# Optimization experiments

Measured on AMD Instinct MI355X. Metric: run time of the kernel, lower is better.

The kernel has to match this reference:

```python
import jax, jax.numpy as jnp
import numpy as np

LN_EPS = 1e-12  # BERT LayerNorm eps


def _layernorm(x, g, b):
    mu = jnp.mean(x, axis=-1, keepdims=True)
    var = jnp.mean(jnp.square(x - mu), axis=-1, keepdims=True)
    return (x - mu) * jax.lax.rsqrt(var + LN_EPS) * g + b


def setup_inputs() -> dict:
    key = jax.random.key(0)
    B, M, D, H, dh, R, Ro, Rf, F = 4, 2048, 768, 12, 64, 32, 256, 256, 3072
    ks = iter(jax.random.split(key, 32))
    n = lambda shape, s=0.02: jax.random.normal(next(ks), shape, jnp.float32) * s
    return {
        'x': jax.random.normal(next(ks), (B, M, D), jnp.float32),
        'mask': jnp.zeros((B, M), jnp.float32),  # HF-style additive mask
        'Pq': n((H, D, R)), 'Vq': n((H, R, dh)), 'bq': n((1, H, 1, dh)),
        'Pk': n((H, D, R)), 'Vk': n((H, R, dh)), 'bk': n((1, H, 1, dh)),
        'Pv': n((H, D, R)), 'Vv': n((H, R, dh)), 'bv': n((1, H, 1, dh)),
        'Uo': n((D, Ro)), 'Vo': n((Ro, D)), 'bo_attn': jnp.zeros((D,), jnp.float32),
        'U1': n((D, Rf)), 'V1': n((Rf, F)), 'b1': jnp.zeros((F,), jnp.float32),
        'U2': n((F, Rf)), 'V2': n((Rf, D)), 'b2': jnp.zeros((D,), jnp.float32),
        'ln1_g': jnp.ones((D,), jnp.float32), 'ln1_b': jnp.zeros((D,), jnp.float32),
        'ln2_g': jnp.ones((D,), jnp.float32), 'ln2_b': jnp.zeros((D,), jnp.float32),
    }


def reference(x, mask, Pq, Vq, bq, Pk, Vk, bk, Pv, Vv, bv,
              Uo, Vo, bo_attn, U1, V1, b1, U2, V2, b2,
              ln1_g, ln1_b, ln2_g, ln2_b):
    B, M, D = x.shape
    H, dh = Pq.shape[0], Vq.shape[2]
    # low-rank per-head Q/K/V: x @ P (bhmr) then @ V (bhmd) + bias
    q = jnp.einsum('bhmr,hrd->bhmd', jnp.einsum('bmd,hdr->bhmr', x, Pq), Vq) + bq
    k = jnp.einsum('bhmr,hrd->bhmd', jnp.einsum('bmd,hdr->bhmr', x, Pk), Vk) + bk
    v = jnp.einsum('bhmr,hrd->bhmd', jnp.einsum('bmd,hdr->bhmr', x, Pv), Vv) + bv
    # attention (flash_svd_attention math: scaled dot-product + additive mask)
    scores = jnp.einsum('bhmd,bhnd->bhmn', q, k) / jnp.sqrt(jnp.float32(dh))
    scores = scores + mask[:, None, None, :]
    attn = jnp.einsum('bhmn,bhnd->bhmd', jax.nn.softmax(scores, axis=-1), v)
    attn = attn.transpose(0, 2, 1, 3).reshape(B, M, D)
    # low-rank output projection + residual + LN1
    x1 = _layernorm(x + (attn @ Uo) @ Vo + bo_attn, ln1_g, ln1_b)
    # low-rank FFN (BERT intermediate: exact GELU)
    mid = x1 @ U1
    y = (jax.nn.gelu(mid @ V1 + b1, approximate=False) @ U2) @ V2 + b2
    return _layernorm(x1 + y, ln2_g, ln2_b)
```

## Files before the change

kernel.cpp:

```cpp
#include <hip/hip_runtime.h>
#include <hip/hip_bf16.h>
#include <math.h>

typedef __hip_bfloat16 bf16;
typedef __attribute__((ext_vector_type(8))) short short8;
typedef __attribute__((ext_vector_type(4))) short short4v;
typedef __attribute__((ext_vector_type(4))) float f32x4;

__device__ __forceinline__ float to_f(float x) { return x; }
__device__ __forceinline__ float to_f(bf16 x) { return __bfloat162float(x); }

template <typename T> __device__ __forceinline__ T from_f(float x);
template <> __device__ __forceinline__ float from_f<float>(float x) { return x; }
template <> __device__ __forceinline__ bf16 from_f<bf16>(float x) { return __float2bfloat16(x); }

__device__ __forceinline__ float gelu_exact(float x) {
    return 0.5f * x * (1.0f + erff(x * 0.70710678118654752f));
}

#define GLD_LDS16(g, l)                                               \
    __builtin_amdgcn_global_load_lds(                                 \
        (const __attribute__((address_space(1))) void*)(g),           \
        (__attribute__((address_space(3))) void*)(l), 16, 0, 0)

__global__ __launch_bounds__(256) void build_w_qkv_lds(const float* __restrict__ Pq,
                                                       const float* __restrict__ Vq,
                                                       const float* __restrict__ Pk,
                                                       const float* __restrict__ Vk,
                                                       const float* __restrict__ Pv,
                                                       const float* __restrict__ Vv,
                                                       bf16* __restrict__ Wt) {
    const int dt = blockIdx.x;
    const int h = blockIdx.y;
    const int which = blockIdx.z;
    const float* P = (which == 0) ? Pq : (which == 1) ? Pk : Pv;
    const float* V = (which == 0) ? Vq : (which == 1) ? Vk : Vv;
    __shared__ __align__(16) float Ps[128][36];
    __shared__ __align__(16) float Vs[32][64];
    __shared__ __align__(16) unsigned int Ot[64][68];
    const int tid = threadIdx.x;

    const float* pbase = P + ((size_t)h * 768 + dt * 128) * 32;
#pragma unroll
    for (int i = 0; i < 4; i++) {
        int idx = tid + i * 256;
        float4 v4 = ((const float4*)pbase)[idx];
        *(float4*)&Ps[idx >> 3][(idx & 7) * 4] = v4;
    }
    const float* vbase = V + (size_t)h * 2048;
#pragma unroll
    for (int i = 0; i < 2; i++) {
        int idx = tid + i * 256;
        ((float4*)&Vs[0][0])[idx] = ((const float4*)vbase)[idx];
    }
    __syncthreads();

    const int e = tid & 63, w = tid >> 6;
    float vreg[32];
#pragma unroll
    for (int r = 0; r < 32; r++) vreg[r] = Vs[r][e];

#pragma unroll
    for (int dp = 0; dp < 16; dp++) {
        const int d0 = w * 32 + dp * 2;
        float a0 = 0.f, a1 = 0.f;
#pragma unroll
        for (int r4 = 0; r4 < 8; r4++) {
            float4 p0 = *(const float4*)&Ps[d0][r4 * 4];
            float4 p1 = *(const float4*)&Ps[d0 + 1][r4 * 4];
            a0 += p0.x * vreg[r4 * 4] + p0.y * vreg[r4 * 4 + 1] + p0.z * vreg[r4 * 4 + 2] + p0.w * vreg[r4 * 4 + 3];
            a1 += p1.x * vreg[r4 * 4] + p1.y * vreg[r4 * 4 + 1] + p1.z * vreg[r4 * 4 + 2] + p1.w * vreg[r4 * 4 + 3];
        }
        unsigned int lo = (unsigned int)(unsigned short)__builtin_bit_cast(short, from_f<bf16>(a0));
        unsigned int hi = (unsigned int)(unsigned short)__builtin_bit_cast(short, from_f<bf16>(a1));
        Ot[e][w * 16 + dp] = lo | (hi << 16);
    }
    __syncthreads();

    const int erow = tid >> 2, c0 = (tid & 3) * 16;
    bf16* dst = Wt + ((size_t)which * 768 + h * 64 + erow) * 768 + dt * 128 + c0 * 2;
    *(uint4*)(dst) = *(const uint4*)&Ot[erow][c0];
    *(uint4*)(dst + 8) = *(const uint4*)&Ot[erow][c0 + 4];
    *(uint4*)(dst + 16) = *(const uint4*)&Ot[erow][c0 + 8];
    *(uint4*)(dst + 24) = *(const uint4*)&Ot[erow][c0 + 12];
}

__global__ __launch_bounds__(256) void cast_transpose_t(const float* __restrict__ in,
                                                        bf16* __restrict__ out,
                                                        int R, int Cc) {
    __shared__ float t[32][33];
    const int r0 = blockIdx.x * 32, c0 = blockIdx.y * 32;
    const int tx = threadIdx.x & 31, ty = threadIdx.x >> 5;
#pragma unroll
    for (int i = 0; i < 4; i++)
        t[ty + i * 8][tx] = in[(size_t)(r0 + ty + i * 8) * Cc + c0 + tx];
    __syncthreads();
#pragma unroll
    for (int i = 0; i < 4; i++)
        out[(size_t)(c0 + ty + i * 8) * R + r0 + tx] = from_f<bf16>(t[tx][ty + i * 8]);
}

__global__ __launch_bounds__(256) void cast_f32_bf16(const float* __restrict__ in,
                                                     bf16* __restrict__ out, int n4) {
    int t = blockIdx.x * 256 + threadIdx.x;
    if (t >= n4) return;
    float4 v = ((const float4*)in)[t];
    bf16 tmp[4] = {from_f<bf16>(v.x), from_f<bf16>(v.y), from_f<bf16>(v.z), from_f<bf16>(v.w)};
    ((short4v*)out)[t] = *(short4v*)tmp;
}

__global__ __launch_bounds__(256) void pack_bias_mask(const float* __restrict__ bq,
                                                      const float* __restrict__ bk,
                                                      const float* __restrict__ bv,
                                                      const float* __restrict__ mask,
                                                      float* __restrict__ bias_out,
                                                      float* __restrict__ mask2) {
    int t = blockIdx.x * 256 + threadIdx.x;
    if (t < 768) {
        bias_out[t] = bq[t];
        bias_out[768 + t] = bk[t];
        bias_out[1536 + t] = bv[t];
    }
    int m = t - 768;
    if (m >= 0 && m < 8192) mask2[m] = mask[m] * 1.44269504088896f;
}

template <typename TOUT, int EPI>
__global__ __launch_bounds__(256) void gemm_mfma(const bf16* __restrict__ A,
                                                 const bf16* __restrict__ Bt,
                                                 const float* __restrict__ bias,
                                                 TOUT* __restrict__ C,
                                                 int M, int N, int K) {
    __shared__ __align__(16) bf16 As[128 * 32];
    __shared__ __align__(16) bf16 Bs[128 * 32];
    const int tid = threadIdx.x;
    const int w = tid >> 6, lane = tid & 63;
    const int l = lane & 15, quad = lane >> 4;
    const int wm = w >> 1, wn = w & 1;
    const int m0 = blockIdx.x * 128, n0 = blockIdx.y * 128;

    const int r_in = lane >> 2;
    const int slot = lane & 3;
    const int rA0 = 2 * w * 16 + r_in, rA1 = rA0 + 16;
    const int q0 = slot ^ ((rA0 >> 1) & 3);
    const int q1 = slot ^ ((rA1 >> 1) & 3);
    const bf16* a0 = A + (size_t)(m0 + rA0) * K + q0 * 8;
    const bf16* a1 = A + (size_t)(m0 + rA1) * K + q1 * 8;
    const bf16* b0 = Bt + (size_t)(n0 + rA0) * K + q0 * 8;
    const bf16* b1 = Bt + (size_t)(n0 + rA1) * K + q1 * 8;
    bf16* lA0 = As + 2 * w * 512;
    bf16* lA1 = lA0 + 512;
    bf16* lB0 = Bs + 2 * w * 512;
    bf16* lB1 = lB0 + 512;

    const int swz = (quad ^ ((l >> 1) & 3)) * 8;
    f32x4 acc[4][4] = {};

    for (int k0 = 0; k0 < K; k0 += 32) {
        GLD_LDS16(a0 + k0, lA0);
        GLD_LDS16(a1 + k0, lA1);
        GLD_LDS16(b0 + k0, lB0);
        GLD_LDS16(b1 + k0, lB1);
        __syncthreads();
        short8 af[4], bfr[4];
#pragma unroll
        for (int mt = 0; mt < 4; mt++)
            af[mt] = *(const short8*)&As[(wm * 64 + mt * 16 + l) * 32 + swz];
#pragma unroll
        for (int nt = 0; nt < 4; nt++)
            bfr[nt] = *(const short8*)&Bs[(wn * 64 + nt * 16 + l) * 32 + swz];
#pragma unroll
        for (int mt = 0; mt < 4; mt++)
#pragma unroll
            for (int nt = 0; nt < 4; nt++)
                acc[mt][nt] = __builtin_amdgcn_mfma_f32_16x16x32_bf16(af[mt], bfr[nt], acc[mt][nt], 0, 0, 0);
        __syncthreads();
    }

    float bs[4];
#pragma unroll
    for (int nt = 0; nt < 4; nt++)
        bs[nt] = bias ? bias[n0 + wn * 64 + nt * 16 + l] : 0.f;
#pragma unroll
    for (int mt = 0; mt < 4; mt++) {
#pragma unroll
        for (int nt = 0; nt < 4; nt++) {
            const int col = n0 + wn * 64 + nt * 16 + l;
#pragma unroll
            for (int r = 0; r < 4; r++) {
                const int row = m0 + wm * 64 + mt * 16 + quad * 4 + r;
                float val = acc[mt][nt][r] + bs[nt];
                if (EPI == 1) val = gelu_exact(val);
                C[(size_t)row * N + col] = from_f<TOUT>(val);
            }
        }
    }
}

template <typename TOUT, int EPI>
__global__ __launch_bounds__(256) void gemm_mfma64(const bf16* __restrict__ A,
                                                   const bf16* __restrict__ Bt,
                                                   const float* __restrict__ bias,
                                                   TOUT* __restrict__ C,
                                                   int M, int N, int K) {
    __shared__ __align__(16) bf16 As[64 * 32];
    __shared__ __align__(16) bf16 Bs[64 * 32];
    const int tid = threadIdx.x;
    const int w = tid >> 6, lane = tid & 63;
    const int l = lane & 15, quad = lane >> 4;
    const int wm = w >> 1, wn = w & 1;
    const int m0 = blockIdx.x * 64, n0 = blockIdx.y * 64;

    const int cid = tid;
    const int srow = cid >> 2, slot = cid & 3;
    const int gq = slot ^ ((srow >> 1) & 3);
    const bf16* ag = A + (size_t)(m0 + srow) * K + gq * 8;
    const bf16* bg = Bt + (size_t)(n0 + srow) * K + gq * 8;
    bf16* lA = As + w * 512;
    bf16* lB = Bs + w * 512;

    f32x4 acc[2][2] = {};

    for (int k0 = 0; k0 < K; k0 += 32) {
        GLD_LDS16(ag + k0, lA);
        GLD_LDS16(bg + k0, lB);
        __syncthreads();
        short8 af[2], bfr[2];
#pragma unroll
        for (int mt = 0; mt < 2; mt++) {
            const int row = wm * 32 + mt * 16 + l;
            af[mt] = *(const short8*)&As[row * 32 + (quad ^ ((row >> 1) & 3)) * 8];
        }
#pragma unroll
        for (int nt = 0; nt < 2; nt++) {
            const int row = wn * 32 + nt * 16 + l;
            bfr[nt] = *(const short8*)&Bs[row * 32 + (quad ^ ((row >> 1) & 3)) * 8];
        }
#pragma unroll
        for (int mt = 0; mt < 2; mt++)
#pragma unroll
            for (int nt = 0; nt < 2; nt++)
                acc[mt][nt] = __builtin_amdgcn_mfma_f32_16x16x32_bf16(af[mt], bfr[nt], acc[mt][nt], 0, 0, 0);
        __syncthreads();
    }

#pragma unroll
    for (int mt = 0; mt < 2; mt++) {
#pragma unroll
        for (int nt = 0; nt < 2; nt++) {
            const int col = n0 + wn * 32 + nt * 16 + l;
            const float bsv = bias ? bias[col] : 0.f;
#pragma unroll
            for (int r = 0; r < 4; r++) {
                const int row = m0 + wm * 32 + mt * 16 + quad * 4 + r;
                float val = acc[mt][nt][r] + bsv;
                if (EPI == 1) val = gelu_exact(val);
                C[(size_t)row * N + col] = from_f<TOUT>(val);
            }
        }
    }
}

__global__ __launch_bounds__(256) void transpose_v(const bf16* __restrict__ qkv,
                                                   bf16* __restrict__ vt) {
    __shared__ __align__(16) bf16 t[64][72];
    const int m0 = blockIdx.x * 64;
    const int h = blockIdx.y;
    const int tid = threadIdx.x;
    const int r = tid >> 2, c0 = (tid & 3) * 16;
    {
        const size_t g = (size_t)(m0 + r) * 2304 + 1536 + h * 64 + c0;
        *(short8*)&t[r][c0] = *(const short8*)(qkv + g);
        *(short8*)&t[r][c0 + 8] = *(const short8*)(qkv + g + 8);
    }
    __syncthreads();
    const int b = m0 >> 11, mm = m0 & 2047;
    const int e = tid >> 2, mi0 = (tid & 3) * 16;
    bf16 tmp[16];
#pragma unroll
    for (int j = 0; j < 16; j++) tmp[j] = t[mi0 + j][e];
    bf16* dst = vt + (((size_t)b * 12 + h) * 64 + e) * 2048 + mm + mi0;
    *(short8*)dst = *(short8*)&tmp[0];
    *(short8*)(dst + 8) = *(short8*)&tmp[8];
}

__global__ __launch_bounds__(256, 4) void flash_attn_mfma(const bf16* __restrict__ qkv,
                                                          const bf16* __restrict__ vt,
                                                          const float* __restrict__ mask2,
                                                          bf16* __restrict__ opart0,
                                                          bf16* __restrict__ opart1,
                                                          float* __restrict__ lpart) {
    const int qt = blockIdx.x, h = blockIdx.y;
    const int b = blockIdx.z >> 1, kh = blockIdx.z & 1;
    const int tid = threadIdx.x;
    const int w = tid >> 6, lane = tid & 63;
    const int l = lane & 15, quad = lane >> 4;

    __shared__ __align__(16) bf16 Ks[2][64 * 64];
    __shared__ __align__(16) bf16 Vs[2][64 * 64];
    __shared__ __align__(16) bf16 Ps[4 * 32 * 64];

    const float C1 = 0.125f * 1.44269504088896f;

    short8 qf[2][2];
#pragma unroll
    for (int mt = 0; mt < 2; mt++) {
        const int qrow = qt * 128 + w * 32 + mt * 16 + l;
        const bf16* qp = qkv + ((size_t)b * 2048 + qrow) * 2304 + h * 64 + quad * 8;
        qf[mt][0] = *(const short8*)qp;
        qf[mt][1] = *(const short8*)(qp + 32);
    }

    short8 ones;
#pragma unroll
    for (int i = 0; i < 8; i++) ones[i] = (short)0x3F80;

    f32x4 of[2][4] = {};
    f32x4 lacc[2] = {};
    bf16* Pw = Ps + w * 2048;

    auto stage = [&](int kc, int buf) {
#pragma unroll
        for (int i = 0; i < 2; i++) {
            const int cid = (w * 2 + i) * 64 + lane;
            const int row = cid >> 3, slot = cid & 7;
            const int gq = slot ^ (row & 7);
            const bf16* kp = qkv + ((size_t)b * 2048 + kc + row) * 2304 + 768 + h * 64 + gq * 8;
            GLD_LDS16(kp, &Ks[buf][(size_t)cid * 8]);
            const bf16* vp = vt + (((size_t)b * 12 + h) * 64 + row) * 2048 + kc + gq * 8;
            GLD_LDS16(vp, &Vs[buf][(size_t)cid * 8]);
        }
    };

    const int kc0 = kh * 1024;
    int cur = 0;
    stage(kc0, 0);

    for (int it = 0; it < 16; it++) {
        const int kc = kc0 + it * 64;
        __syncthreads();
        float4 mrow[4];
#pragma unroll
        for (int nt = 0; nt < 4; nt++)
            mrow[nt] = *(const float4*)&mask2[(size_t)b * 2048 + kc + nt * 16 + quad * 4];
        if (it < 15) stage(kc + 64, cur ^ 1);

        const bf16* Kc = Ks[cur];
        const bf16* Vc = Vs[cur];

        f32x4 st[2][4];
#pragma unroll
        for (int nt = 0; nt < 4; nt++) {
            const int rb = (nt * 16 + l) * 64;
            short8 kf0 = *(const short8*)&Kc[rb + ((quad) ^ (l & 7)) * 8];
            short8 kf1 = *(const short8*)&Kc[rb + ((4 + quad) ^ (l & 7)) * 8];
#pragma unroll
            for (int mt = 0; mt < 2; mt++) {
                f32x4 a = {};
                a = __builtin_amdgcn_mfma_f32_16x16x32_bf16(kf0, qf[mt][0], a, 0, 0, 0);
                a = __builtin_amdgcn_mfma_f32_16x16x32_bf16(kf1, qf[mt][1], a, 0, 0, 0);
                st[mt][nt] = a;
            }
        }

#pragma unroll
        for (int mt = 0; mt < 2; mt++) {
#pragma unroll
            for (int nt = 0; nt < 4; nt++) {
                const float* mg = (const float*)&mrow[nt];
                float p0 = exp2f(fmaf(st[mt][nt][0], C1, mg[0]));
                float p1 = exp2f(fmaf(st[mt][nt][1], C1, mg[1]));
                float p2 = exp2f(fmaf(st[mt][nt][2], C1, mg[2]));
                float p3 = exp2f(fmaf(st[mt][nt][3], C1, mg[3]));
                unsigned d0 = __builtin_amdgcn_perm(__builtin_bit_cast(unsigned, p1),
                                                    __builtin_bit_cast(unsigned, p0), 0x07060302u);
                unsigned d1 = __builtin_amdgcn_perm(__builtin_bit_cast(unsigned, p3),
                                                    __builtin_bit_cast(unsigned, p2), 0x07060302u);
                const int slot8 = (2 * nt + (quad >> 1)) ^ (l & 7);
                uint2 u = {d0, d1};
                *(uint2*)&Pw[(mt * 16 + l) * 64 + slot8 * 8 + (quad & 1) * 4] = u;
            }
        }

        short8 pa[2][2];
#pragma unroll
        for (int mt = 0; mt < 2; mt++)
#pragma unroll
            for (int ks = 0; ks < 2; ks++)
                pa[mt][ks] = *(const short8*)&Pw[(mt * 16 + l) * 64 + ((ks * 4 + quad) ^ (l & 7)) * 8];

#pragma unroll
        for (int mt = 0; mt < 2; mt++) {
            lacc[mt] = __builtin_amdgcn_mfma_f32_16x16x32_bf16(pa[mt][0], ones, lacc[mt], 0, 0, 0);
            lacc[mt] = __builtin_amdgcn_mfma_f32_16x16x32_bf16(pa[mt][1], ones, lacc[mt], 0, 0, 0);
        }

#pragma unroll
        for (int nt = 0; nt < 4; nt++) {
            const int rb = (nt * 16 + l) * 64;
            short8 vf0 = *(const short8*)&Vc[rb + ((quad) ^ (l & 7)) * 8];
            short8 vf1 = *(const short8*)&Vc[rb + ((4 + quad) ^ (l & 7)) * 8];
#pragma unroll
            for (int mt = 0; mt < 2; mt++) {
                of[mt][nt] = __builtin_amdgcn_mfma_f32_16x16x32_bf16(pa[mt][0], vf0, of[mt][nt], 0, 0, 0);
                of[mt][nt] = __builtin_amdgcn_mfma_f32_16x16x32_bf16(pa[mt][1], vf1, of[mt][nt], 0, 0, 0);
            }
        }
        cur ^= 1;
    }

#pragma unroll
    for (int mt = 0; mt < 2; mt++) {
        if (l == 0) {
#pragma unroll
            for (int r = 0; r < 4; r++)
                lpart[(((size_t)kh * 4 + b) * 12 + h) * 2048 + qt * 128 + w * 32 + mt * 16 + quad * 4 + r] =
                    lacc[mt][r];
        }
    }

    bf16* op = kh ? opart1 : opart0;
#pragma unroll
    for (int mt = 0; mt < 2; mt++) {
#pragma unroll
        for (int r = 0; r < 4; r++) {
            const int row = qt * 128 + w * 32 + mt * 16 + quad * 4 + r;
#pragma unroll
            for (int nt = 0; nt < 4; nt++)
                op[((size_t)b * 2048 + row) * 768 + h * 64 + nt * 16 + l] =
                    from_f<bf16>(of[mt][nt][r]);
        }
    }
}

__global__ __launch_bounds__(256) void attn_combine(const bf16* __restrict__ o0,
                                                    const bf16* __restrict__ o1,
                                                    const float* __restrict__ lp,
                                                    bf16* __restrict__ outp) {
    const int t = blockIdx.x * 256 + threadIdx.x;
    const int col4 = t % 192;
    const int row = t / 192;
    const int b = row >> 11, m = row & 2047;
    const int h = col4 >> 4;
    const float l0 = lp[((size_t)b * 12 + h) * 2048 + m];
    const float l1 = lp[((size_t)(4 + b) * 12 + h) * 2048 + m];
    const float iv = 1.f / (l0 + l1);
    short4v a = ((const short4v*)o0)[t];
    short4v c = ((const short4v*)o1)[t];
    bf16 r[4];
#pragma unroll
    for (int i = 0; i < 4; i++) {
        float f = to_f(__builtin_bit_cast(bf16, a[i])) + to_f(__builtin_bit_cast(bf16, c[i]));
        r[i] = from_f<bf16>(f * iv);
    }
    ((short4v*)outp)[t] = *(short4v*)r;
}

template <typename TIN, typename TADD, typename TOUT>
__global__ __launch_bounds__(256) void ln_kernel(const TIN* __restrict__ base,
                                                 const TADD* __restrict__ add,
                                                 const float* __restrict__ gamma,
                                                 const float* __restrict__ beta,
                                                 TOUT* __restrict__ out) {
    const int row = blockIdx.x;
    const int tid = threadIdx.x;
    __shared__ float red[4];
    const size_t o = (size_t)row * 768;
    float v[3];
#pragma unroll
    for (int i = 0; i < 3; i++) {
        int d = tid + i * 256;
        v[i] = to_f(base[o + d]) + to_f(add[o + d]);
    }
    float s = v[0] + v[1] + v[2];
#pragma unroll
    for (int off = 32; off > 0; off >>= 1) s += __shfl_down(s, off, 64);
    const int wave = tid >> 6, lane = tid & 63;
    if (lane == 0) red[wave] = s;
    __syncthreads();
    float mu = (red[0] + red[1] + red[2] + red[3]) * (1.0f / 768.0f);
    float d0 = v[0] - mu, d1 = v[1] - mu, d2 = v[2] - mu;
    float sq = d0 * d0 + d1 * d1 + d2 * d2;
    __syncthreads();
#pragma unroll
    for (int off = 32; off > 0; off >>= 1) sq += __shfl_down(sq, off, 64);
    if (lane == 0) red[wave] = sq;
    __syncthreads();
    float var = (red[0] + red[1] + red[2] + red[3]) * (1.0f / 768.0f);
    float rs = rsqrtf(var + 1e-12f);
#pragma unroll
    for (int i = 0; i < 3; i++) {
        int d = tid + i * 256;
        float y = (v[i] - mu) * rs * gamma[d] + beta[d];
        out[o + d] = from_f<TOUT>(y);
    }
}

extern "C" void kernel_launch(void* const* d_in, const int* in_sizes, int n_in,
                              void* d_out, int out_size, void* d_ws, size_t ws_size,
                              hipStream_t stream) {
    const float* x    = (const float*)d_in[0];
    const float* mask = (const float*)d_in[1];
    const float* Pq = (const float*)d_in[2];
    const float* Vq = (const float*)d_in[3];
    const float* bq = (const float*)d_in[4];
    const float* Pk = (const float*)d_in[5];
    const float* Vk = (const float*)d_in[6];
    const float* bk = (const float*)d_in[7];
    const float* Pv = (const float*)d_in[8];
    const float* Vv = (const float*)d_in[9];
    const float* bv = (const float*)d_in[10];
    const float* Uo = (const float*)d_in[11];
    const float* Vo = (const float*)d_in[12];
    const float* bo = (const float*)d_in[13];
    const float* U1 = (const float*)d_in[14];
    const float* V1 = (const float*)d_in[15];
    const float* b1 = (const float*)d_in[16];
    const float* U2 = (const float*)d_in[17];
    const float* V2 = (const float*)d_in[18];
    const float* b2 = (const float*)d_in[19];
    const float* g1 = (const float*)d_in[20];
    const float* be1 = (const float*)d_in[21];
    const float* g2 = (const float*)d_in[22];
    const float* be2 = (const float*)d_in[23];

    char* p = (char*)d_ws;
    bf16* Wqkv_t = (bf16*)p;            p += (size_t)2304 * 768 * 2;
    bf16* Wo_t   = (bf16*)p;            p += (size_t)768 * 768 * 2;
    bf16* U1t    = (bf16*)p;            p += (size_t)256 * 768 * 2;
    bf16* V1t    = (bf16*)p;            p += (size_t)3072 * 256 * 2;
    bf16* U2t    = (bf16*)p;            p += (size_t)256 * 3072 * 2;
    bf16* V2t    = (bf16*)p;            p += (size_t)768 * 256 * 2;
    float* bias_qkv = (float*)p;        p += (size_t)2304 * 4;
    float* mask2 = (float*)p;           p += (size_t)8192 * 4;
    bf16* xb     = (bf16*)p;
    bf16* x1b    = xb;                  p += (size_t)8192 * 768 * 2;
    bf16* qkv    = (bf16*)p;
    bf16* gbuf   = qkv;                 p += (size_t)8192 * 2304 * 2;
    bf16* vtb    = (bf16*)p;            p += (size_t)8192 * 768 * 2;
    bf16* attnb  = (bf16*)p;
    bf16* t2     = attnb;               p += (size_t)8192 * 768 * 2;
    char* regR   = p;                   p += (size_t)8192 * 768 * 4;
    bf16* t1     = (bf16*)p;            p += (size_t)8192 * 256 * 2;
    bf16* Vot = (bf16*)regR;
    bf16* Uob = Vot + (size_t)768 * 256;
    bf16* opart1 = (bf16*)regR;
    float* lpart = (float*)(regR + (size_t)8192 * 768 * 2);
    bf16* y1b = (bf16*)regR;
    bf16* y2b = (bf16*)(regR + (size_t)8192 * 768 * 2);

    build_w_qkv_lds<<<dim3(6, 12, 3), 256, 0, stream>>>(Pq, Vq, Pk, Vk, Pv, Vv, Wqkv_t);
    cast_transpose_t<<<dim3(8, 24), 256, 0, stream>>>(Vo, Vot, 256, 768);
    cast_f32_bf16<<<192, 256, 0, stream>>>(Uo, Uob, 768 * 256 / 4);
    gemm_mfma<bf16, 0><<<dim3(6, 6), 256, 0, stream>>>(Vot, Uob, nullptr, Wo_t, 768, 768, 256);
    cast_transpose_t<<<dim3(24, 8), 256, 0, stream>>>(U1, U1t, 768, 256);
    cast_transpose_t<<<dim3(8, 96), 256, 0, stream>>>(V1, V1t, 256, 3072);
    cast_transpose_t<<<dim3(96, 8), 256, 0, stream>>>(U2, U2t, 3072, 256);
    cast_transpose_t<<<dim3(8, 24), 256, 0, stream>>>(V2, V2t, 256, 768);
    pack_bias_mask<<<35, 256, 0, stream>>>(bq, bk, bv, mask, bias_qkv, mask2);
    cast_f32_bf16<<<6144, 256, 0, stream>>>(x, xb, 8192 * 768 / 4);

    gemm_mfma<bf16, 0><<<dim3(64, 18), 256, 0, stream>>>(xb, Wqkv_t, bias_qkv, qkv, 8192, 2304, 768);

    transpose_v<<<dim3(128, 12), 256, 0, stream>>>(qkv, vtb);

    flash_attn_mfma<<<dim3(16, 12, 8), 256, 0, stream>>>(qkv, vtb, mask2, attnb, opart1, lpart);
    attn_combine<<<6144, 256, 0, stream>>>(attnb, opart1, lpart, attnb);

    gemm_mfma<bf16, 0><<<dim3(64, 6), 256, 0, stream>>>(attnb, Wo_t, bo, y1b, 8192, 768, 768);

    ln_kernel<float, bf16, bf16><<<8192, 256, 0, stream>>>(x, y1b, g1, be1, x1b);

    gemm_mfma64<bf16, 0><<<dim3(128, 4), 256, 0, stream>>>(x1b, U1t, nullptr, t1, 8192, 256, 768);

    gemm_mfma<bf16, 1><<<dim3(64, 24), 256, 0, stream>>>(t1, V1t, b1, gbuf, 8192, 3072, 256);

    gemm_mfma64<bf16, 0><<<dim3(128, 4), 256, 0, stream>>>(gbuf, U2t, nullptr, t2, 8192, 256, 3072);

    gemm_mfma<bf16, 0><<<dim3(64, 6), 256, 0, stream>>>(t2, V2t, b2, y2b, 8192, 768, 256);

    ln_kernel<bf16, bf16, float><<<8192, 256, 0, stream>>>(x1b, y2b, g2, be2, (float*)d_out);
}
```

Baseline: 430.6 us.

## Fold softmax scale into Q weights, batch weight transposes, trim attention overhead

```diff
diff --git a/kernel.cpp b/kernel.cpp
--- a/kernel.cpp
+++ b/kernel.cpp
@@ -6,6 +6,9 @@
 typedef __attribute__((ext_vector_type(8))) short short8;
 typedef __attribute__((ext_vector_type(4))) short short4v;
 typedef __attribute__((ext_vector_type(4))) float f32x4;
+
+#define C1F 0.18033688011112042f
+#define LOG2E 1.44269504088896f
 
 __device__ __forceinline__ float to_f(float x) { return x; }
 __device__ __forceinline__ float to_f(bf16 x) { return __bfloat162float(x); }
@@ -35,6 +38,7 @@
     const int which = blockIdx.z;
     const float* P = (which == 0) ? Pq : (which == 1) ? Pk : Pv;
     const float* V = (which == 0) ? Vq : (which == 1) ? Vk : Vv;
+    const float scale = (which == 0) ? C1F : 1.0f;
     __shared__ __align__(16) float Ps[128][36];
     __shared__ __align__(16) float Vs[32][64];
     __shared__ __align__(16) unsigned int Ot[64][68];
@@ -71,6 +75,8 @@
             a0 += p0.x * vreg[r4 * 4] + p0.y * vreg[r4 * 4 + 1] + p0.z * vreg[r4 * 4 + 2] + p0.w * vreg[r4 * 4 + 3];
             a1 += p1.x * vreg[r4 * 4] + p1.y * vreg[r4 * 4 + 1] + p1.z * vreg[r4 * 4 + 2] + p1.w * vreg[r4 * 4 + 3];
         }
+        a0 *= scale;
+        a1 *= scale;
         unsigned int lo = (unsigned int)(unsigned short)__builtin_bit_cast(short, from_f<bf16>(a0));
         unsigned int hi = (unsigned int)(unsigned short)__builtin_bit_cast(short, from_f<bf16>(a1));
         Ot[e][w * 16 + dp] = lo | (hi << 16);
@@ -85,19 +91,44 @@
     *(uint4*)(dst + 24) = *(const uint4*)&Ot[erow][c0 + 12];
 }
 
+__device__ __forceinline__ void ct_tile(const float* in, bf16* out, int R, int Cc,
+                                        int r0, int c0, int tx, int ty) {
+    __shared__ float t[32][33];
+#pragma unroll
+    for (int i = 0; i < 4; i++)
+        t[ty + i * 8][tx] = in[(size_t)(r0 + ty + i * 8) * Cc + c0 + tx];
+    __syncthreads();
+#pragma unroll
+    for (int i = 0; i < 4; i++)
+        out[(size_t)(c0 + ty + i * 8) * R + r0 + tx] = from_f<bf16>(t[tx][ty + i * 8]);
+}
+
 __global__ __launch_bounds__(256) void cast_transpose_t(const float* __restrict__ in,
                                                         bf16* __restrict__ out,
                                                         int R, int Cc) {
-    __shared__ float t[32][33];
-    const int r0 = blockIdx.x * 32, c0 = blockIdx.y * 32;
-    const int tx = threadIdx.x & 31, ty = threadIdx.x >> 5;
-#pragma unroll
-    for (int i = 0; i < 4; i++)
-        t[ty + i * 8][tx] = in[(size_t)(r0 + ty + i * 8) * Cc + c0 + tx];
-    __syncthreads();
-#pragma unroll
-    for (int i = 0; i < 4; i++)
-        out[(size_t)(c0 + ty + i * 8) * R + r0 + tx] = from_f<bf16>(t[tx][ty + i * 8]);
+    ct_tile(in, out, R, Cc, blockIdx.x * 32, blockIdx.y * 32,
+            threadIdx.x & 31, threadIdx.x >> 5);
+}
+
+__global__ __launch_bounds__(256) void cast_transpose_batch(const float* __restrict__ U1,
+                                                            const float* __restrict__ V1,
+                                                            const float* __restrict__ U2,
+                                                            const float* __restrict__ V2,
+                                                            bf16* __restrict__ U1t,
+                                                            bf16* __restrict__ V1t,
+                                                            bf16* __restrict__ U2t,
+                                                            bf16* __restrict__ V2t) {
+    int t = blockIdx.x;
+    const float* in;
+    bf16* out;
+    int R, Cc;
+    if (t < 192) { in = U1; out = U1t; R = 768; Cc = 256; }
+    else if (t < 960) { t -= 192; in = V1; out = V1t; R = 256; Cc = 3072; }
+    else if (t < 1728) { t -= 960; in = U2; out = U2t; R = 3072; Cc = 256; }
+    else { t -= 1728; in = V2; out = V2t; R = 256; Cc = 768; }
+    const int tpr = Cc >> 5;
+    ct_tile(in, out, R, Cc, (t / tpr) * 32, (t % tpr) * 32,
+            threadIdx.x & 31, threadIdx.x >> 5);
 }
 
 __global__ __launch_bounds__(256) void cast_f32_bf16(const float* __restrict__ in,
@@ -117,12 +148,12 @@
                                                       float* __restrict__ mask2) {
     int t = blockIdx.x * 256 + threadIdx.x;
     if (t < 768) {
-        bias_out[t] = bq[t];
+        bias_out[t] = bq[t] * C1F;
         bias_out[768 + t] = bk[t];
         bias_out[1536 + t] = bv[t];
     }
     int m = t - 768;
-    if (m >= 0 && m < 8192) mask2[m] = mask[m] * 1.44269504088896f;
+    if (m >= 0 && m < 8192) mask2[m] = mask[m] * LOG2E;
 }
 
 template <typename TOUT, int EPI>
@@ -298,9 +329,7 @@
 
     __shared__ __align__(16) bf16 Ks[2][64 * 64];
     __shared__ __align__(16) bf16 Vs[2][64 * 64];
-    __shared__ __align__(16) bf16 Ps[4 * 32 * 64];
-
-    const float C1 = 0.125f * 1.44269504088896f;
+    __shared__ __align__(16) bf16 Ps[4 * 16 * 64];
 
     short8 qf[2][2];
 #pragma unroll
@@ -317,33 +346,45 @@
 
     f32x4 of[2][4] = {};
     f32x4 lacc[2] = {};
-    bf16* Pw = Ps + w * 2048;
-
-    auto stage = [&](int kc, int buf) {
+    bf16* Pw = Ps + w * 1024;
+
+    const int kc0 = kh * 1024;
+    int cids[2], ldst[2];
+    const bf16* kg[2];
+    const bf16* vg[2];
+#pragma unroll
+    for (int i = 0; i < 2; i++) {
+        const int cid = (w * 2 + i) * 64 + lane;
+        const int row = cid >> 3, slot = cid & 7;
+        const int gq = slot ^ (row & 7);
+        cids[i] = cid;
+        ldst[i] = cid * 8;
+        kg[i] = qkv + ((size_t)b * 2048 + kc0 + row) * 2304 + 768 + h * 64 + gq * 8;
+        vg[i] = vt + (((size_t)b * 12 + h) * 64 + row) * 2048 + kc0 + gq * 8;
+    }
+    const float* mp = mask2 + (size_t)b * 2048 + kc0 + quad * 4;
+
+    auto stage = [&](int buf) {
 #pragma unroll
         for (int i = 0; i < 2; i++) {
-            const int cid = (w * 2 + i) * 64 + lane;
-            const int row = cid >> 3, slot = cid & 7;
-            const int gq = slot ^ (row & 7);
-            const bf16* kp = qkv + ((size_t)b * 2048 + kc + row) * 2304 + 768 + h * 64 + gq * 8;
-            GLD_LDS16(kp, &Ks[buf][(size_t)cid * 8]);
-            const bf16* vp = vt + (((size_t)b * 12 + h) * 64 + row) * 2048 + kc + gq * 8;
-            GLD_LDS16(vp, &Vs[buf][(size_t)cid * 8]);
+            GLD_LDS16(kg[i], &Ks[buf][ldst[i]]);
+            GLD_LDS16(vg[i], &Vs[buf][ldst[i]]);
+            kg[i] += 64 * 2304;
+            vg[i] += 64;
         }
     };
 
-    const int kc0 = kh * 1024;
     int cur = 0;
-    stage(kc0, 0);
-
+    stage(0);
+
+#pragma unroll 2
     for (int it = 0; it < 16; it++) {
-        const int kc = kc0 + it * 64;
         __syncthreads();
         float4 mrow[4];
 #pragma unroll
-        for (int nt = 0; nt < 4; nt++)
-            mrow[nt] = *(const float4*)&mask2[(size_t)b * 2048 + kc + nt * 16 + quad * 4];
-        if (it < 15) stage(kc + 64, cur ^ 1);
+        for (int nt = 0; nt < 4; nt++) mrow[nt] = *(const float4*)(mp + nt * 16);
+        mp += 64;
+        if (it < 15) stage(cur ^ 1);
 
         const bf16* Kc = Ks[cur];
         const bf16* Vc = Vs[cur];
@@ -356,38 +397,34 @@
             short8 kf1 = *(const short8*)&Kc[rb + ((4 + quad) ^ (l & 7)) * 8];
 #pragma unroll
             for (int mt = 0; mt < 2; mt++) {
-                f32x4 a = {};
+                f32x4 a = {mrow[nt].x, mrow[nt].y, mrow[nt].z, mrow[nt].w};
                 a = __builtin_amdgcn_mfma_f32_16x16x32_bf16(kf0, qf[mt][0], a, 0, 0, 0);
                 a = __builtin_amdgcn_mfma_f32_16x16x32_bf16(kf1, qf[mt][1], a, 0, 0, 0);
                 st[mt][nt] = a;
             }
         }
 
+        short8 pa[2][2];
 #pragma unroll
         for (int mt = 0; mt < 2; mt++) {
 #pragma unroll
             for (int nt = 0; nt < 4; nt++) {
-                const float* mg = (const float*)&mrow[nt];
-                float p0 = exp2f(fmaf(st[mt][nt][0], C1, mg[0]));
-                float p1 = exp2f(fmaf(st[mt][nt][1], C1, mg[1]));
-                float p2 = exp2f(fmaf(st[mt][nt][2], C1, mg[2]));
-                float p3 = exp2f(fmaf(st[mt][nt][3], C1, mg[3]));
+                float p0 = exp2f(st[mt][nt][0]);
+                float p1 = exp2f(st[mt][nt][1]);
+                float p2 = exp2f(st[mt][nt][2]);
+                float p3 = exp2f(st[mt][nt][3]);
                 unsigned d0 = __builtin_amdgcn_perm(__builtin_bit_cast(unsigned, p1),
                                                     __builtin_bit_cast(unsigned, p0), 0x07060302u);
                 unsigned d1 = __builtin_amdgcn_perm(__builtin_bit_cast(unsigned, p3),
                                                     __builtin_bit_cast(unsigned, p2), 0x07060302u);
                 const int slot8 = (2 * nt + (quad >> 1)) ^ (l & 7);
                 uint2 u = {d0, d1};
-                *(uint2*)&Pw[(mt * 16 + l) * 64 + slot8 * 8 + (quad & 1) * 4] = u;
+                *(uint2*)&Pw[l * 64 + slot8 * 8 + (quad & 1) * 4] = u;
             }
-        }
-
-        short8 pa[2][2];
-#pragma unroll
-        for (int mt = 0; mt < 2; mt++)
 #pragma unroll
             for (int ks = 0; ks < 2; ks++)
-                pa[mt][ks] = *(const short8*)&Pw[(mt * 16 + l) * 64 + ((ks * 4 + quad) ^ (l & 7)) * 8];
+                pa[mt][ks] = *(const short8*)&Pw[l * 64 + ((ks * 4 + quad) ^ (l & 7)) * 8];
+        }
 
 #pragma unroll
         for (int mt = 0; mt < 2; mt++) {
@@ -553,10 +590,7 @@
     cast_transpose_t<<<dim3(8, 24), 256, 0, stream>>>(Vo, Vot, 256, 768);
     cast_f32_bf16<<<192, 256, 0, stream>>>(Uo, Uob, 768 * 256 / 4);
     gemm_mfma<bf16, 0><<<dim3(6, 6), 256, 0, stream>>>(Vot, Uob, nullptr, Wo_t, 768, 768, 256);
-    cast_transpose_t<<<dim3(24, 8), 256, 0, stream>>>(U1, U1t, 768, 256);
-    cast_transpose_t<<<dim3(8, 96), 256, 0, stream>>>(V1, V1t, 256, 3072);
-    cast_transpose_t<<<dim3(96, 8), 256, 0, stream>>>(U2, U2t, 3072, 256);
-    cast_transpose_t<<<dim3(8, 24), 256, 0, stream>>>(V2, V2t, 256, 768);
+    cast_transpose_batch<<<1920, 256, 0, stream>>>(U1, V1, U2, V2, U1t, V1t, U2t, V2t);
     pack_bias_mask<<<35, 256, 0, stream>>>(bq, bk, bv, mask, bias_qkv, mask2);
     cast_f32_bf16<<<6144, 256, 0, stream>>>(x, xb, 8192 * 768 / 4);
 
@@ -569,7 +603,7 @@
 
     gemm_mfma<bf16, 0><<<dim3(64, 6), 256, 0, stream>>>(attnb, Wo_t, bo, y1b, 8192, 768, 768);
 
-    ln_kernel<float, bf16, bf16><<<8192, 256, 0, stream>>>(x, y1b, g1, be1, x1b);
+    ln_kernel<bf16, bf16, bf16><<<8192, 256, 0, stream>>>(xb, y1b, g1, be1, x1b);
 
     gemm_mfma64<bf16, 0><<<dim3(128, 4), 256, 0, stream>>>(x1b, U1t, nullptr, t1, 8192, 256, 768);
 
```

New measurement: 420.9 us. 2.2% less time.
